# Performance work log

Hardware: AMD Instinct MI355X
Metric: run time of the kernel (lower is better)

## Reference

```python
import jax, jax.numpy as jnp
import numpy as np

NODE_DIM = 128
EDGE_ATTR_DIM = 64
OUT_DIM = 128
N_NODES = 10000
N_EDGES = 640000


def setup_inputs() -> dict:
    key = jax.random.key(0)
    k1, k2, k3, k4, k5, k6, k7 = jax.random.split(key, 7)
    x = jax.random.normal(k1, (N_NODES, NODE_DIM), dtype=jnp.float32)
    edge_index = jax.random.randint(k2, (2, N_EDGES), 0, N_NODES, dtype=jnp.int64)
    edge_attr = jax.random.normal(k3, (N_EDGES, EDGE_ATTR_DIM), dtype=jnp.float32)
    in_dim = 2 * NODE_DIM + EDGE_ATTR_DIM  # 320
    s1 = 1.0 / np.sqrt(in_dim)
    s2 = 1.0 / np.sqrt(OUT_DIM)
    W1 = jax.random.uniform(k4, (in_dim, OUT_DIM), jnp.float32, -s1, s1)
    b1 = jax.random.uniform(k5, (OUT_DIM,), jnp.float32, -s1, s1)
    W2 = jax.random.uniform(k6, (OUT_DIM, OUT_DIM), jnp.float32, -s2, s2)
    b2 = jax.random.uniform(k7, (OUT_DIM,), jnp.float32, -s2, s2)
    return {"x": x, "edge_index": edge_index, "edge_attr": edge_attr,
            "W1": W1, "b1": b1, "W2": W2, "b2": b2}


def reference(x, edge_index, edge_attr, W1, b1, W2, b2):
    src, tgt = edge_index[0], edge_index[1]
    x_i = x[src]                      # [E, node_dim] gather
    x_j = x[tgt]                      # [E, node_dim] gather
    edge_input = jnp.concatenate([x_i, x_j, edge_attr], axis=1)  # [E, 320]
    h = jax.nn.relu(edge_input @ W1 + b1)   # [E, out_dim]
    return h @ W2 + b2                      # [E, out_dim]
```

## Files before the change

### kernel.cpp

```cpp
#include <hip/hip_runtime.h>


typedef __bf16 bf16;
typedef __attribute__((ext_vector_type(8)))  __bf16 bf16x8;
typedef __attribute__((ext_vector_type(4)))  float  f32x4;
typedef __attribute__((ext_vector_type(16))) float  f32x16;

#define N_EDGES 640000
#define BM      64
#define NTHR    256

__global__ void prep_weights(const float* __restrict__ W1, const float* __restrict__ W2,
                             bf16* __restrict__ w1f, bf16* __restrict__ w2f) {
    int i = blockIdx.x * 256 + threadIdx.x;
    if (i < 40960) {
        int j = i & 7, l = (i >> 3) & 63, q = i >> 9;
        int ks = q % 20, nt = q / 20;
        int n = nt * 32 + (l & 31);
        int k = ks * 16 + ((l >> 5) << 3) + j;
        w1f[i] = (bf16)W1[k * 128 + n];
    } else if (i < 40960 + 16384) {
        int i2 = i - 40960;
        int j = i2 & 7, l = (i2 >> 3) & 63, q = i2 >> 9;
        int ks = q & 7, nt = q >> 3;
        int n = nt * 32 + (l & 31);
        int k = ks * 16 + ((l >> 5) << 3) + j;
        w2f[i2] = (bf16)W2[k * 128 + n];
    }
}

__global__ __launch_bounds__(NTHR, 2) void edge_mlp(
    const float* __restrict__ x, const int* __restrict__ eidx,
    const float* __restrict__ eattr, const bf16* __restrict__ w1f,
    const float* __restrict__ b1, const bf16* __restrict__ w2f,
    const float* __restrict__ b2, float* __restrict__ out)
{
    extern __shared__ char smem[];
    bf16* sA = (bf16*)smem;
    char* sH = smem + 40960;

    const int tid   = threadIdx.x;
    const int wave  = tid >> 6;
    const int lane  = tid & 63;
    const int ebase = blockIdx.x * BM;

#pragma unroll
    for (int i = 0; i < 10; ++i) {
        const int slot = i * NTHR + tid;
        const int blk  = slot >> 6;
        const int sub  = slot & 63;
        const int mt   = blk / 20;
        const int ks   = blk % 20;
        const int m    = mt * 32 + (sub & 31);
        const int k    = ks * 16 + ((sub >> 5) << 3);
        f32x4 v0, v1;
        if (ks < 8) {
            const f32x4* p = (const f32x4*)(x + (size_t)eidx[ebase + m] * 128 + k);
            v0 = p[0]; v1 = p[1];
        } else if (ks < 16) {
            const f32x4* p = (const f32x4*)(x + (size_t)eidx[N_EDGES + ebase + m] * 128 + (k - 128));
            v0 = p[0]; v1 = p[1];
        } else {
            const f32x4* p = (const f32x4*)(eattr + (size_t)(ebase + m) * 64 + (k - 256));
            v0 = __builtin_nontemporal_load(p);
            v1 = __builtin_nontemporal_load(p + 1);
        }
        bf16x8 bv;
        bv[0] = (bf16)v0.x; bv[1] = (bf16)v0.y; bv[2] = (bf16)v0.z; bv[3] = (bf16)v0.w;
        bv[4] = (bf16)v1.x; bv[5] = (bf16)v1.y; bv[6] = (bf16)v1.z; bv[7] = (bf16)v1.w;
        *(bf16x8*)&sA[slot * 8] = bv;
    }

    bf16x8 w1r[20];
    {
        const bf16x8* wp = (const bf16x8*)w1f + (wave * 20 * 64 + lane);
#pragma unroll
        for (int ks = 0; ks < 20; ++ks) w1r[ks] = wp[ks * 64];
    }

    f32x16 acc0, acc1;
#pragma unroll
    for (int i = 0; i < 16; ++i) { acc0[i] = 0.f; acc1[i] = 0.f; }

    __syncthreads();

    __builtin_amdgcn_s_setprio(1);
#pragma unroll
    for (int ks = 0; ks < 20; ++ks) {
        bf16x8 a0 = *(const bf16x8*)&sA[((0 * 20 + ks) * 64 + lane) * 8];
        bf16x8 a1 = *(const bf16x8*)&sA[((1 * 20 + ks) * 64 + lane) * 8];
        acc0 = __builtin_amdgcn_mfma_f32_32x32x16_bf16(a0, w1r[ks], acc0, 0, 0, 0);
        acc1 = __builtin_amdgcn_mfma_f32_32x32x16_bf16(a1, w1r[ks], acc1, 0, 0, 0);
    }
    __builtin_amdgcn_s_setprio(0);

    bf16x8 w2r[8];
    {
        const bf16x8* wp = (const bf16x8*)w2f + (wave * 8 * 64 + lane);
#pragma unroll
        for (int ks = 0; ks < 8; ++ks) w2r[ks] = wp[ks * 64];
    }

    {
        const int   ln   = lane & 31;
        const int   kn   = wave * 32 + ln;
        const int   rowq = (lane >> 5) << 2;
        const float b1v  = b1[kn];
        const int   colb = ((kn >> 4) * 64 + ((kn >> 3) & 1) * 32) * 16 + (kn & 7) * 2;
        const int   kx   = ((kn >> 3) & 7) << 5;
#pragma unroll
        for (int r = 0; r < 16; ++r) {
            const int ml  = (r & 3) + ((r >> 2) << 3) + rowq;
            const int off = colb + ml * 16;
            *(bf16*)(sH + ((off       ) ^ kx)) = (bf16)fmaxf(acc0[r] + b1v, 0.f);
            *(bf16*)(sH + ((off + 8192) ^ kx)) = (bf16)fmaxf(acc1[r] + b1v, 0.f);
        }
    }
    __syncthreads();

#pragma unroll
    for (int i = 0; i < 16; ++i) { acc0[i] = 0.f; acc1[i] = 0.f; }
    __builtin_amdgcn_s_setprio(1);
#pragma unroll
    for (int ks = 0; ks < 8; ++ks) {
        int o0 = ((0 * 8 + ks) * 64 + lane) * 16;
        int o1 = ((1 * 8 + ks) * 64 + lane) * 16;
        o0 ^= ((o0 >> 9) & 7) << 5;
        o1 ^= ((o1 >> 9) & 7) << 5;
        bf16x8 a0 = *(const bf16x8*)(sH + o0);
        bf16x8 a1 = *(const bf16x8*)(sH + o1);
        acc0 = __builtin_amdgcn_mfma_f32_32x32x16_bf16(a0, w2r[ks], acc0, 0, 0, 0);
        acc1 = __builtin_amdgcn_mfma_f32_32x32x16_bf16(a1, w2r[ks], acc1, 0, 0, 0);
    }
    __builtin_amdgcn_s_setprio(0);

    {
        const int   ln   = lane & 31;
        const int   n    = wave * 32 + ln;
        const int   rowq = (lane >> 5) << 2;
        const float b2v  = b2[n];
#pragma unroll
        for (int r = 0; r < 16; ++r) {
            const int ml = (r & 3) + ((r >> 2) << 3) + rowq;
            __builtin_nontemporal_store(acc0[r] + b2v, &out[(size_t)(ebase      + ml) * 128 + n]);
            __builtin_nontemporal_store(acc1[r] + b2v, &out[(size_t)(ebase + 32 + ml) * 128 + n]);
        }
    }
}

extern "C" void kernel_launch(void* const* d_in, const int* in_sizes, int n_in,
                              void* d_out, int out_size, void* d_ws, size_t ws_size,
                              hipStream_t stream) {
    const float* x   = (const float*)d_in[0];
    const int*   ei  = (const int*)d_in[1];
    const float* ea  = (const float*)d_in[2];
    const float* W1  = (const float*)d_in[3];
    const float* b1  = (const float*)d_in[4];
    const float* W2  = (const float*)d_in[5];
    const float* b2  = (const float*)d_in[6];
    float*       out = (float*)d_out;

    bf16* w1f = (bf16*)d_ws;
    bf16* w2f = (bf16*)((char*)d_ws + 81920);

    prep_weights<<<224, 256, 0, stream>>>(W1, W2, w1f, w2f);

    const size_t shmem = 40960 + 16384;
    edge_mlp<<<N_EDGES / BM, NTHR, shmem, stream>>>(x, ei, ea, w1f, b1, w2f, b2, out);
}
```

Before: 620.6 us.

## Make edge MLP kernel persistent with software-pipelined gather prefetch

Changes the one-tile-per-block launch into 512 persistent blocks, each looping over a contiguous run of 64-edge tiles. Weights stay in registers across tiles, and all edge indices for the block are staged in LDS up front. The next tile's gathered rows are loaded into registers during the current tile's MFMAs and written to LDS in two halves. This is meant to hide gather latency and cut per-block setup. The cost is more registers, extra LDS for indices, and more barriers per tile. With 512 blocks the grid may only partly fill a 256-CU device at two blocks per CU.

```diff
diff --git a/kernel.cpp b/kernel.cpp
--- a/kernel.cpp
+++ b/kernel.cpp
@@ -9,6 +9,10 @@
 #define N_EDGES 640000
 #define BM      64
 #define NTHR    256
+#define NBLK    512
+#define TILES   (N_EDGES / BM)
+#define TPB     (TILES / NBLK)
+#define TREM    (TILES % NBLK)
 
 __global__ void prep_weights(const float* __restrict__ W1, const float* __restrict__ W2,
                              bf16* __restrict__ w1f, bf16* __restrict__ w2f) {
@@ -29,6 +33,33 @@
     }
 }
 
+#define STG_ISSUE(g, tloc, d0, d1) {                                                  \
+    const int blk_ = (g) * 4 + wave;                                                  \
+    const int mq_  = (blk_ >= 20) ? 1 : 0;                                            \
+    const int ks_  = blk_ - mq_ * 20;                                                 \
+    const int m_   = mq_ * 32 + (lane & 31);                                          \
+    const int kh_  = (lane >> 5) << 3;                                                \
+    if (ks_ < 8) {                                                                    \
+        const f32x4* p_ = (const f32x4*)(x + (size_t)sIdx[(tloc)*128 + m_] * 128      \
+                                           + ks_ * 16 + kh_);                         \
+        d0 = p_[0]; d1 = p_[1];                                                       \
+    } else if (ks_ < 16) {                                                            \
+        const f32x4* p_ = (const f32x4*)(x + (size_t)sIdx[(tloc)*128 + 64 + m_] * 128 \
+                                           + (ks_ - 8) * 16 + kh_);                   \
+        d0 = p_[0]; d1 = p_[1];                                                       \
+    } else {                                                                          \
+        const f32x4* p_ = (const f32x4*)(eattr + ((size_t)(tbase + (tloc)) * 64 + m_) * 64 \
+                                           + (ks_ - 16) * 16 + kh_);                  \
+        d0 = __builtin_nontemporal_load(p_);                                          \
+        d1 = __builtin_nontemporal_load(p_ + 1);                                      \
+    } }
+
+#define STG_WRITE(g, d0, d1) {                                                        \
+    bf16x8 bv_;                                                                       \
+    bv_[0] = (bf16)d0.x; bv_[1] = (bf16)d0.y; bv_[2] = (bf16)d0.z; bv_[3] = (bf16)d0.w; \
+    bv_[4] = (bf16)d1.x; bv_[5] = (bf16)d1.y; bv_[6] = (bf16)d1.z; bv_[7] = (bf16)d1.w; \
+    *(bf16x8*)&sA[((g) * NTHR + tid) * 8] = bv_; }
+
 __global__ __launch_bounds__(NTHR, 2) void edge_mlp(
     const float* __restrict__ x, const int* __restrict__ eidx,
     const float* __restrict__ eattr, const bf16* __restrict__ w1f,
@@ -36,39 +67,22 @@
     const float* __restrict__ b2, float* __restrict__ out)
 {
     extern __shared__ char smem[];
-    bf16* sA = (bf16*)smem;
-    char* sH = smem + 40960;
+    bf16* sA   = (bf16*)smem;
+    char* sH   = smem + 40960;
+    int*  sIdx = (int*)(smem + 40960 + 16384);
 
     const int tid   = threadIdx.x;
     const int wave  = tid >> 6;
     const int lane  = tid & 63;
-    const int ebase = blockIdx.x * BM;
-
-#pragma unroll
-    for (int i = 0; i < 10; ++i) {
-        const int slot = i * NTHR + tid;
-        const int blk  = slot >> 6;
-        const int sub  = slot & 63;
-        const int mt   = blk / 20;
-        const int ks   = blk % 20;
-        const int m    = mt * 32 + (sub & 31);
-        const int k    = ks * 16 + ((sub >> 5) << 3);
-        f32x4 v0, v1;
-        if (ks < 8) {
-            const f32x4* p = (const f32x4*)(x + (size_t)eidx[ebase + m] * 128 + k);
-            v0 = p[0]; v1 = p[1];
-        } else if (ks < 16) {
-            const f32x4* p = (const f32x4*)(x + (size_t)eidx[N_EDGES + ebase + m] * 128 + (k - 128));
-            v0 = p[0]; v1 = p[1];
-        } else {
-            const f32x4* p = (const f32x4*)(eattr + (size_t)(ebase + m) * 64 + (k - 256));
-            v0 = __builtin_nontemporal_load(p);
-            v1 = __builtin_nontemporal_load(p + 1);
-        }
-        bf16x8 bv;
-        bv[0] = (bf16)v0.x; bv[1] = (bf16)v0.y; bv[2] = (bf16)v0.z; bv[3] = (bf16)v0.w;
-        bv[4] = (bf16)v1.x; bv[5] = (bf16)v1.y; bv[6] = (bf16)v1.z; bv[7] = (bf16)v1.w;
-        *(bf16x8*)&sA[slot * 8] = bv;
+    const int b     = blockIdx.x;
+    const int count = TPB + (b < TREM ? 1 : 0);
+    const int tbase = b * TPB + (b < TREM ? b : TREM);
+
+    const int nE = count * BM;
+    for (int i = tid; i < nE; i += NTHR) {
+        const int tt = i >> 6, m = i & 63;
+        sIdx[tt * 128 + m]      = eidx[tbase * BM + i];
+        sIdx[tt * 128 + 64 + m] = eidx[N_EDGES + tbase * BM + i];
     }
 
     bf16x8 w1r[20];
@@ -77,37 +91,64 @@
 #pragma unroll
         for (int ks = 0; ks < 20; ++ks) w1r[ks] = wp[ks * 64];
     }
-
-    f32x16 acc0, acc1;
-#pragma unroll
-    for (int i = 0; i < 16; ++i) { acc0[i] = 0.f; acc1[i] = 0.f; }
-
-    __syncthreads();
-
-    __builtin_amdgcn_s_setprio(1);
-#pragma unroll
-    for (int ks = 0; ks < 20; ++ks) {
-        bf16x8 a0 = *(const bf16x8*)&sA[((0 * 20 + ks) * 64 + lane) * 8];
-        bf16x8 a1 = *(const bf16x8*)&sA[((1 * 20 + ks) * 64 + lane) * 8];
-        acc0 = __builtin_amdgcn_mfma_f32_32x32x16_bf16(a0, w1r[ks], acc0, 0, 0, 0);
-        acc1 = __builtin_amdgcn_mfma_f32_32x32x16_bf16(a1, w1r[ks], acc1, 0, 0, 0);
-    }
-    __builtin_amdgcn_s_setprio(0);
-
     bf16x8 w2r[8];
     {
         const bf16x8* wp = (const bf16x8*)w2f + (wave * 8 * 64 + lane);
 #pragma unroll
         for (int ks = 0; ks < 8; ++ks) w2r[ks] = wp[ks * 64];
     }
+    const int   kn   = wave * 32 + (lane & 31);
+    const int   rowq = (lane >> 5) << 2;
+    const float b1v  = b1[kn];
+    const float b2v  = b2[kn];
+    const int   colb = ((kn >> 4) * 64 + ((kn >> 3) & 1) * 32) * 16 + (kn & 7) * 2;
+    const int   kx   = ((kn >> 3) & 7) << 5;
+
+    __syncthreads();
 
     {
-        const int   ln   = lane & 31;
-        const int   kn   = wave * 32 + ln;
-        const int   rowq = (lane >> 5) << 2;
-        const float b1v  = b1[kn];
-        const int   colb = ((kn >> 4) * 64 + ((kn >> 3) & 1) * 32) * 16 + (kn & 7) * 2;
-        const int   kx   = ((kn >> 3) & 7) << 5;
+        f32x4 p0[5], p1[5];
+#pragma unroll
+        for (int g = 0; g < 5; ++g) STG_ISSUE(g, 0, p0[g], p1[g]);
+#pragma unroll
+        for (int g = 0; g < 5; ++g) STG_WRITE(g, p0[g], p1[g]);
+#pragma unroll
+        for (int g = 5; g < 10; ++g) STG_ISSUE(g, 0, p0[g - 5], p1[g - 5]);
+#pragma unroll
+        for (int g = 5; g < 10; ++g) STG_WRITE(g, p0[g - 5], p1[g - 5]);
+    }
+    __syncthreads();
+
+    for (int t = 0; t < count; ++t) {
+        const bool pf = (t + 1 < count);
+        f32x4 p0[5], p1[5];
+
+        if (pf) {
+#pragma unroll
+            for (int g = 0; g < 5; ++g) STG_ISSUE(g, t + 1, p0[g], p1[g]);
+        }
+
+        f32x16 acc0, acc1;
+#pragma unroll
+        for (int i = 0; i < 16; ++i) { acc0[i] = 0.f; acc1[i] = 0.f; }
+        __builtin_amdgcn_s_setprio(1);
+#pragma unroll
+        for (int ks = 0; ks < 20; ++ks) {
+            bf16x8 a0 = *(const bf16x8*)&sA[((     ks) * 64 + lane) * 8];
+            bf16x8 a1 = *(const bf16x8*)&sA[((20 + ks) * 64 + lane) * 8];
+            acc0 = __builtin_amdgcn_mfma_f32_32x32x16_bf16(a0, w1r[ks], acc0, 0, 0, 0);
+            acc1 = __builtin_amdgcn_mfma_f32_32x32x16_bf16(a1, w1r[ks], acc1, 0, 0, 0);
+        }
+        __builtin_amdgcn_s_setprio(0);
+        __syncthreads();
+
+        if (pf) {
+#pragma unroll
+            for (int g = 0; g < 5; ++g) STG_WRITE(g, p0[g], p1[g]);
+#pragma unroll
+            for (int g = 5; g < 10; ++g) STG_ISSUE(g, t + 1, p0[g - 5], p1[g - 5]);
+        }
+
 #pragma unroll
         for (int r = 0; r < 16; ++r) {
             const int ml  = (r & 3) + ((r >> 2) << 3) + rowq;
@@ -115,36 +156,39 @@
             *(bf16*)(sH + ((off       ) ^ kx)) = (bf16)fmaxf(acc0[r] + b1v, 0.f);
             *(bf16*)(sH + ((off + 8192) ^ kx)) = (bf16)fmaxf(acc1[r] + b1v, 0.f);
         }
-    }
-    __syncthreads();
-
-#pragma unroll
-    for (int i = 0; i < 16; ++i) { acc0[i] = 0.f; acc1[i] = 0.f; }
-    __builtin_amdgcn_s_setprio(1);
-#pragma unroll
-    for (int ks = 0; ks < 8; ++ks) {
-        int o0 = ((0 * 8 + ks) * 64 + lane) * 16;
-        int o1 = ((1 * 8 + ks) * 64 + lane) * 16;
-        o0 ^= ((o0 >> 9) & 7) << 5;
-        o1 ^= ((o1 >> 9) & 7) << 5;
-        bf16x8 a0 = *(const bf16x8*)(sH + o0);
-        bf16x8 a1 = *(const bf16x8*)(sH + o1);
-        acc0 = __builtin_amdgcn_mfma_f32_32x32x16_bf16(a0, w2r[ks], acc0, 0, 0, 0);
-        acc1 = __builtin_amdgcn_mfma_f32_32x32x16_bf16(a1, w2r[ks], acc1, 0, 0, 0);
-    }
-    __builtin_amdgcn_s_setprio(0);
-
-    {
-        const int   ln   = lane & 31;
-        const int   n    = wave * 32 + ln;
-        const int   rowq = (lane >> 5) << 2;
-        const float b2v  = b2[n];
-#pragma unroll
-        for (int r = 0; r < 16; ++r) {
-            const int ml = (r & 3) + ((r >> 2) << 3) + rowq;
-            __builtin_nontemporal_store(acc0[r] + b2v, &out[(size_t)(ebase      + ml) * 128 + n]);
-            __builtin_nontemporal_store(acc1[r] + b2v, &out[(size_t)(ebase + 32 + ml) * 128 + n]);
-        }
+        __syncthreads();
+
+#pragma unroll
+        for (int i = 0; i < 16; ++i) { acc0[i] = 0.f; acc1[i] = 0.f; }
+        __builtin_amdgcn_s_setprio(1);
+#pragma unroll
+        for (int ks = 0; ks < 8; ++ks) {
+            int o0 = ((     ks) * 64 + lane) * 16;
+            int o1 = ((8 +  ks) * 64 + lane) * 16;
+            o0 ^= ((o0 >> 9) & 7) << 5;
+            o1 ^= ((o1 >> 9) & 7) << 5;
+            bf16x8 a0 = *(const bf16x8*)(sH + o0);
+            bf16x8 a1 = *(const bf16x8*)(sH + o1);
+            acc0 = __builtin_amdgcn_mfma_f32_32x32x16_bf16(a0, w2r[ks], acc0, 0, 0, 0);
+            acc1 = __builtin_amdgcn_mfma_f32_32x32x16_bf16(a1, w2r[ks], acc1, 0, 0, 0);
+        }
+        __builtin_amdgcn_s_setprio(0);
+
+        {
+            const size_t ebase = (size_t)(tbase + t) * BM;
+#pragma unroll
+            for (int r = 0; r < 16; ++r) {
+                const int ml = (r & 3) + ((r >> 2) << 3) + rowq;
+                __builtin_nontemporal_store(acc0[r] + b2v, &out[(ebase      + ml) * 128 + kn]);
+                __builtin_nontemporal_store(acc1[r] + b2v, &out[(ebase + 32 + ml) * 128 + kn]);
+            }
+        }
+
+        if (pf) {
+#pragma unroll
+            for (int g = 5; g < 10; ++g) STG_WRITE(g, p0[g - 5], p1[g - 5]);
+        }
+        __syncthreads();
     }
 }
 
@@ -165,6 +209,6 @@
 
     prep_weights<<<224, 256, 0, stream>>>(W1, W2, w1f, w2f);
 
-    const size_t shmem = 40960 + 16384;
-    edge_mlp<<<N_EDGES / BM, NTHR, shmem, stream>>>(x, ei, ea, w1f, b1, w2f, b2, out);
+    const size_t shmem = 40960 + 16384 + 10240;
+    edge_mlp<<<NBLK, NTHR, shmem, stream>>>(x, ei, ea, w1f, b1, w2f, b2, out);
 }
```

Measured after the change: 579.5 us. -6.6%, faster.
